# Kernel optimization log

Hardware: AMD Instinct MI355X
Metric: run time of the kernel (lower is better)

Reference implementation:

```python
import jax, jax.numpy as jnp
import numpy as np

GRID_SIZE = 5
SPLINE_ORDER = 3
GRID_MIN, GRID_MAX = -1.0, 1.0
LN_EPS = 1e-5


def _make_grid():
    # Extended knot grid shared across input features: (grid_size + 2*order + 1,)
    h = (GRID_MAX - GRID_MIN) / GRID_SIZE
    return jnp.arange(-SPLINE_ORDER, GRID_SIZE + SPLINE_ORDER + 1, dtype=jnp.float32) * h + GRID_MIN


def b_splines(x, grid):
    # x: (B, in) -> bases: (B, in, grid_size + spline_order)
    xe = x[..., None]  # (B, in, 1)
    bases = ((xe >= grid[:-1]) & (xe < grid[1:])).astype(x.dtype)
    for k in range(1, SPLINE_ORDER + 1):
        left = (xe - grid[: -(k + 1)]) / (grid[k:-1] - grid[: -(k + 1)])
        right = (grid[k + 1:] - xe) / (grid[k + 1:] - grid[1:-k])
        bases = left * bases[..., :-1] + right * bases[..., 1:]
    return bases


def setup_inputs() -> dict:
    key = jax.random.key(0)
    ks = jax.random.split(key, 5)
    B, IN, OUT, COEF = 16384, 1024, 512, GRID_SIZE + SPLINE_ORDER
    return {
        "rgb_features": jax.random.normal(ks[0], (B, IN // 2), jnp.float32),
        "tactile_features": jax.random.normal(ks[1], (B, IN // 2), jnp.float32),
        "base_weight": jax.random.normal(ks[2], (OUT, IN), jnp.float32) * 0.02,
        "spline_weight": jax.random.normal(ks[3], (OUT, IN, COEF), jnp.float32) * 0.02,
        "spline_scaler": 1.0 + 0.02 * jax.random.normal(ks[4], (OUT, IN), jnp.float32),
        "ln_gamma": jnp.ones((OUT,), jnp.float32),
        "ln_beta": jnp.zeros((OUT,), jnp.float32),
    }


def reference(rgb_features, tactile_features, base_weight, spline_weight, spline_scaler, ln_gamma, ln_beta):
    x = jnp.concatenate((rgb_features, tactile_features), axis=1)  # (B, 1024)
    grid = _make_grid()
    # KANLinear: base path (SiLU + linear) + spline path (B-spline basis + linear)
    base_out = jnp.einsum("bi,oi->bo", jax.nn.silu(x), base_weight)
    bases = b_splines(x, grid)  # (B, in, coef)
    scaled_w = spline_weight * spline_scaler[..., None]  # (out, in, coef)
    spline_out = jnp.einsum("bik,oik->bo", bases, scaled_w)
    fused = base_out + spline_out
    # LayerNorm over last dim
    mu = jnp.mean(fused, axis=-1, keepdims=True)
    var = jnp.var(fused, axis=-1, keepdims=True)
    fused = (fused - mu) * jax.lax.rsqrt(var + LN_EPS) * ln_gamma + ln_beta
    # Dropout is identity in eval mode
    return fused
```

## Files before the change

kernel.cpp:

```cpp
#include <hip/hip_runtime.h>
#include <cstdint>
#include <cstddef>


#define BATCH    16384
#define OUT_DIM  512
#define KTOT     9216
#define BM       128
#define BK       64
#define NCHUNK        144
#define SPLINE_CHUNKS 128

typedef __attribute__((ext_vector_type(8))) short  short8;
typedef __attribute__((ext_vector_type(4))) float  f32x4;

static __device__ __forceinline__ unsigned short f2bf(float f) {
    unsigned int u = __float_as_uint(f);
    unsigned int r = u + 0x7fffu + ((u >> 16) & 1u);
    return (unsigned short)(r >> 16);
}

__global__ void prep_w_kernel(const float* __restrict__ bw,
                              const float* __restrict__ sw,
                              const float* __restrict__ sc,
                              unsigned short* __restrict__ Wp) {
    int t = blockIdx.x * 256 + threadIdx.x;
    int o = t / 1152;
    int g = t - o * 1152;
    int sz = o & 7;
    unsigned short o8[8];
    size_t dst;
    if (g < 1024) {
        float s = sc[(size_t)o * 1024 + g];
        const float* w = sw + ((size_t)o * 1024 + g) * 8;
        #pragma unroll
        for (int k = 0; k < 8; ++k) o8[k] = f2bf(w[k] * s);
        dst = (size_t)o * KTOT + (size_t)(g >> 3) * 64 + (size_t)(((g & 7) ^ sz)) * 8;
    } else {
        int gi = g - 1024;
        const float* w = bw + (size_t)o * 1024 + gi * 8;
        #pragma unroll
        for (int k = 0; k < 8; ++k) o8[k] = f2bf(w[k]);
        dst = (size_t)o * KTOT + (size_t)8192 + (size_t)(gi >> 3) * 64 + (size_t)(((gi & 7) ^ sz)) * 8;
    }
    *reinterpret_cast<short8*>(Wp + dst) = *reinterpret_cast<const short8*>(o8);
}

static __device__ __forceinline__ void basis8(float x, unsigned* out) {
    float tpos = (x + 2.2f) * 2.5f;
    float fj   = floorf(tpos);
    int   j    = (int)fj;
    float u  = tpos - fj;
    float v  = 1.f - u;
    float u2 = u * u;
    float u3 = u2 * u;
    const float c6 = 1.f / 6.f;
    float n0 = v * v * v * c6;
    float n1 = (3.f * u3 - 6.f * u2 + 4.f) * c6;
    float n2 = (-3.f * u3 + 3.f * u2 + 3.f * u + 1.f) * c6;
    float n3 = u3 * c6;
    unsigned p0, p1;
    asm("v_cvt_pk_bf16_f32 %0, %1, %2" : "=v"(p0) : "v"(n0), "v"(n1));
    asm("v_cvt_pk_bf16_f32 %0, %1, %2" : "=v"(p1) : "v"(n2), "v"(n3));
    int sh = (j << 4) - 48;
    int c  = sh & 16;
    int w  = (sh - c) >> 5;
    unsigned long long P = ((unsigned long long)p1 << 32) | p0;
    unsigned long long T = P << c;
    unsigned t0 = (unsigned)T;
    unsigned t1 = (unsigned)(T >> 32);
    unsigned t2 = c ? (p1 >> 16) : 0u;
    #pragma unroll
    for (int i = 0; i < 4; ++i) {
        unsigned r = 0u;
        r = (w == i    ) ? t0 : r;
        r = (w == i - 1) ? t1 : r;
        r = (w == i - 2) ? t2 : r;
        out[i] = r;
    }
}

template<bool SPLIT>
__launch_bounds__(1024, 4)
__global__ void kan_gemm_kernel(const float* __restrict__ rgb,
                                const float* __restrict__ tac,
                                const unsigned short* __restrict__ Wp,
                                float* __restrict__ dest_base) {
    __shared__ unsigned short At[2][BM][BK];
    __shared__ unsigned short Bt[2][OUT_DIM][BK];

    const int tid  = threadIdx.x;
    const int lane = tid & 63;
    const int wid  = tid >> 6;
    const int b0   = blockIdx.x * BM;
    const int wr   = wid & 1;
    const int wc   = wid >> 1;
    const int ksp  = SPLIT ? (int)blockIdx.y : 0;
    const int kc0  = SPLIT ? (ksp ? 72 : 0)             : 0;
    const int kcS  = SPLIT ? (ksp ? SPLINE_CHUNKS : 72) : SPLINE_CHUNKS;
    const int kc1  = SPLIT ? (ksp ? NCHUNK : 72)        : NCHUNK;
    float* dest = dest_base + (size_t)ksp * BATCH * OUT_DIM;

    const int ar  = tid >> 3;
    const int af_ = tid & 7;

    f32x4 acc[4][4];
    #pragma unroll
    for (int m = 0; m < 4; ++m)
        #pragma unroll
        for (int n = 0; n < 4; ++n)
            acc[m][n] = (f32x4){0.f, 0.f, 0.f, 0.f};

    auto mfma_step = [&](int ab, int bb) {
        #pragma unroll
        for (int ks = 0; ks < 2; ++ks) {
            int cb = ks * 4 + (lane >> 4);
            short8 afr[4];
            #pragma unroll
            for (int m = 0; m < 4; ++m) {
                int row = wr * 64 + m * 16 + (lane & 15);
                afr[m] = *reinterpret_cast<const short8*>(&At[ab][row][(cb ^ (row & 7)) * 8]);
            }
            #pragma unroll
            for (int n = 0; n < 4; ++n) {
                int row = wc * 64 + n * 16 + (lane & 15);
                short8 bfr = *reinterpret_cast<const short8*>(
                    &Bt[bb][row][(cb ^ (row & 7)) * 8]);
                #pragma unroll
                for (int m = 0; m < 4; ++m)
                    acc[m][n] = __builtin_amdgcn_mfma_f32_16x16x32_bf16(
                        afr[m], bfr, acc[m][n], 0, 0, 0);
            }
        }
    };

    auto loadx_s = [&](int c) -> float {
        int i0 = c * 8;
        const float* xs = (i0 < 512) ? rgb : tac;
        int ic = i0 & 511;
        return xs[(size_t)(b0 + ar) * 512 + ic + af_];
    };

    auto loadx_b = [&](int c, f32x4& xa, f32x4& xb) {
        int i0 = (c - SPLINE_CHUNKS) * 64;
        const float* xs = (i0 < 512) ? rgb : tac;
        int ic = i0 & 511;
        const float* xp = xs + (size_t)(b0 + ar) * 512 + ic + af_ * 8;
        xa = *reinterpret_cast<const f32x4*>(xp);
        xb = *reinterpret_cast<const f32x4*>(xp + 4);
    };

    auto silupack = [&](const f32x4& xa, const f32x4& xb, unsigned* o) {
        float s[8];
        #pragma unroll
        for (int q = 0; q < 4; ++q) {
            float a = xa[q]; s[q]     = a / (1.f + __expf(-a));
            float b = xb[q]; s[q + 4] = b / (1.f + __expf(-b));
        }
        #pragma unroll
        for (int q = 0; q < 4; ++q)
            asm("v_cvt_pk_bf16_f32 %0, %1, %2"
                : "=v"(o[q]) : "v"(s[2 * q]), "v"(s[2 * q + 1]));
    };

    auto writeA = [&](const unsigned* o4, int ab) {
        *reinterpret_cast<short8*>(&At[ab][ar][(af_ ^ (ar & 7)) * 8]) =
            *reinterpret_cast<const short8*>(o4);
    };

    auto gload_B = [&](int kc, int buf) {
        int k0g = kc * BK;
        #pragma unroll
        for (int rp = 0; rp < 4; ++rp) {
            int row0 = wid * 32 + rp * 8;
            const unsigned short* gp =
                Wp + (size_t)(row0 + (lane >> 3)) * KTOT + k0g + (lane & 7) * 8;
            __builtin_amdgcn_global_load_lds(
                (const __attribute__((address_space(1))) unsigned int*)gp,
                (__attribute__((address_space(3))) unsigned int*)&Bt[buf][row0][0],
                16, 0, 0);
        }
    };

    gload_B(kc0, 0);
    gload_B(kc0 + 1 < kc1 ? kc0 + 1 : kc1 - 1, 1);
    {
        float x0 = loadx_s(kc0);
        unsigned o4[4];
        basis8(x0, o4);
        writeA(o4, 0);
    }
    float xn = (kc0 + 1 < kcS) ? loadx_s(kc0 + 1) : 0.f;
    asm volatile("s_waitcnt vmcnt(4) lgkmcnt(0)" ::: "memory");
    __builtin_amdgcn_sched_barrier(0);
    __builtin_amdgcn_s_barrier();
    __builtin_amdgcn_sched_barrier(0);

    for (int t = kc0; t < kcS; ++t) {
        const int  buf   = (t - kc0) & 1;
        const bool moreA = (t + 1 < kcS);
        unsigned o4[4];
        if (moreA) {
            basis8(xn, o4);
            writeA(o4, buf ^ 1);
        }
        if (t + 2 < kcS) xn = loadx_s(t + 2);
        mfma_step(buf, buf);
        __builtin_amdgcn_sched_barrier(0);
        __builtin_amdgcn_s_barrier();
        __builtin_amdgcn_sched_barrier(0);
        int tn = (t + 2 < kc1) ? t + 2 : kc1 - 1;
        gload_B(tn, buf);
        asm volatile("s_waitcnt vmcnt(4) lgkmcnt(0)" ::: "memory");
        __builtin_amdgcn_sched_barrier(0);
        __builtin_amdgcn_s_barrier();
        __builtin_amdgcn_sched_barrier(0);
    }

    if (kcS < kc1) {
        f32x4 xa{}, xb{};
        {
            f32x4 a0, b0;
            loadx_b(kcS, a0, b0);
            unsigned o4[4];
            silupack(a0, b0, o4);
            writeA(o4, (kcS - kc0) & 1);
            if (kcS + 1 < kc1) loadx_b(kcS + 1, xa, xb);
            asm volatile("s_waitcnt lgkmcnt(0)" ::: "memory");
            __builtin_amdgcn_sched_barrier(0);
            __builtin_amdgcn_s_barrier();
            __builtin_amdgcn_sched_barrier(0);
        }
        for (int t = kcS; t < kc1; ++t) {
            const int  buf   = (t - kc0) & 1;
            const bool moreA = (t + 1 < kc1);
            unsigned o4[4];
            if (moreA) {
                silupack(xa, xb, o4);
                writeA(o4, buf ^ 1);
            }
            f32x4 na, nb;
            const bool moreX = (t + 2 < kc1);
            if (moreX) loadx_b(t + 2, na, nb);
            mfma_step(buf, buf);
            __builtin_amdgcn_sched_barrier(0);
            __builtin_amdgcn_s_barrier();
            __builtin_amdgcn_sched_barrier(0);
            int tn = moreX ? t + 2 : kc1 - 1;
            gload_B(tn, buf);
            asm volatile("s_waitcnt vmcnt(4) lgkmcnt(0)" ::: "memory");
            __builtin_amdgcn_sched_barrier(0);
            __builtin_amdgcn_s_barrier();
            __builtin_amdgcn_sched_barrier(0);
            if (moreX) { xa = na; xb = nb; }
        }
    }

    #pragma unroll
    for (int m = 0; m < 4; ++m) {
        int row = b0 + wr * 64 + m * 16 + ((lane >> 4) << 2);
        #pragma unroll
        for (int n = 0; n < 4; ++n) {
            int col = wc * 64 + n * 16 + (lane & 15);
            #pragma unroll
            for (int jj = 0; jj < 4; ++jj)
                dest[(size_t)(row + jj) * OUT_DIM + col] = acc[m][n][jj];
        }
    }
}

__global__ void reduce_ln_kernel(const float* __restrict__ P0,
                                 const float* __restrict__ P1,
                                 const float* __restrict__ gamma,
                                 const float* __restrict__ beta,
                                 float* __restrict__ out) {
    int row  = blockIdx.x * 4 + (threadIdx.x >> 6);
    int lane = threadIdx.x & 63;
    const float* p0 = P0 + (size_t)row * OUT_DIM;
    const float* p1 = P1 + (size_t)row * OUT_DIM;
    f32x4 a0 = *reinterpret_cast<const f32x4*>(p0 + lane * 4);
    f32x4 a1 = *reinterpret_cast<const f32x4*>(p0 + 256 + lane * 4);
    f32x4 b0 = *reinterpret_cast<const f32x4*>(p1 + lane * 4);
    f32x4 b1 = *reinterpret_cast<const f32x4*>(p1 + 256 + lane * 4);
    f32x4 v0, v1;
    #pragma unroll
    for (int q = 0; q < 4; ++q) { v0[q] = a0[q] + b0[q]; v1[q] = a1[q] + b1[q]; }
    float s = 0.f, ss = 0.f;
    #pragma unroll
    for (int q = 0; q < 4; ++q) {
        s  += v0[q] + v1[q];
        ss += v0[q] * v0[q] + v1[q] * v1[q];
    }
    #pragma unroll
    for (int off = 1; off < 64; off <<= 1) {
        s  += __shfl_xor(s, off);
        ss += __shfl_xor(ss, off);
    }
    float mu  = s * (1.f / 512.f);
    float var = ss * (1.f / 512.f) - mu * mu;
    float rs  = rsqrtf(var + 1e-5f);
    f32x4 g0 = *reinterpret_cast<const f32x4*>(gamma + lane * 4);
    f32x4 g1 = *reinterpret_cast<const f32x4*>(gamma + 256 + lane * 4);
    f32x4 e0 = *reinterpret_cast<const f32x4*>(beta + lane * 4);
    f32x4 e1 = *reinterpret_cast<const f32x4*>(beta + 256 + lane * 4);
    float* po = out + (size_t)row * OUT_DIM;
    f32x4 r0, r1;
    #pragma unroll
    for (int q = 0; q < 4; ++q) {
        r0[q] = (v0[q] - mu) * rs * g0[q] + e0[q];
        r1[q] = (v1[q] - mu) * rs * g1[q] + e1[q];
    }
    *reinterpret_cast<f32x4*>(po + lane * 4)       = r0;
    *reinterpret_cast<f32x4*>(po + 256 + lane * 4) = r1;
}

__global__ void ln_kernel(float* __restrict__ io,
                          const float* __restrict__ gamma,
                          const float* __restrict__ beta) {
    int row  = blockIdx.x * 4 + (threadIdx.x >> 6);
    int lane = threadIdx.x & 63;
    float* p = io + (size_t)row * OUT_DIM;
    f32x4 v0 = *reinterpret_cast<const f32x4*>(p + lane * 4);
    f32x4 v1 = *reinterpret_cast<const f32x4*>(p + 256 + lane * 4);
    float s = 0.f, ss = 0.f;
    #pragma unroll
    for (int q = 0; q < 4; ++q) {
        s  += v0[q] + v1[q];
        ss += v0[q] * v0[q] + v1[q] * v1[q];
    }
    #pragma unroll
    for (int off = 1; off < 64; off <<= 1) {
        s  += __shfl_xor(s, off);
        ss += __shfl_xor(ss, off);
    }
    float mu  = s * (1.f / 512.f);
    float var = ss * (1.f / 512.f) - mu * mu;
    float rs  = rsqrtf(var + 1e-5f);
    f32x4 g0 = *reinterpret_cast<const f32x4*>(gamma + lane * 4);
    f32x4 g1 = *reinterpret_cast<const f32x4*>(gamma + 256 + lane * 4);
    f32x4 e0 = *reinterpret_cast<const f32x4*>(beta + lane * 4);
    f32x4 e1 = *reinterpret_cast<const f32x4*>(beta + 256 + lane * 4);
    f32x4 r0, r1;
    #pragma unroll
    for (int q = 0; q < 4; ++q) {
        r0[q] = (v0[q] - mu) * rs * g0[q] + e0[q];
        r1[q] = (v1[q] - mu) * rs * g1[q] + e1[q];
    }
    *reinterpret_cast<f32x4*>(p + lane * 4)       = r0;
    *reinterpret_cast<f32x4*>(p + 256 + lane * 4) = r1;
}

extern "C" void kernel_launch(void* const* d_in, const int* in_sizes, int n_in,
                              void* d_out, int out_size, void* d_ws, size_t ws_size,
                              hipStream_t stream) {
    const float* rgb   = (const float*)d_in[0];
    const float* tac   = (const float*)d_in[1];
    const float* bw    = (const float*)d_in[2];
    const float* sw    = (const float*)d_in[3];
    const float* sc    = (const float*)d_in[4];
    const float* gamma = (const float*)d_in[5];
    const float* beta  = (const float*)d_in[6];
    float* out = (float*)d_out;
    unsigned short* Wp = (unsigned short*)d_ws;

    prep_w_kernel<<<2304, 256, 0, stream>>>(bw, sw, sc, Wp);

    const size_t PART = (size_t)BATCH * OUT_DIM * sizeof(float);
    const size_t POFF = 16ull << 20;
    if (ws_size >= POFF + 2 * PART) {
        float* P = (float*)((char*)d_ws + POFF);
        dim3 g(BATCH / BM, 2);
        kan_gemm_kernel<true><<<g, 1024, 0, stream>>>(rgb, tac, Wp, P);
        reduce_ln_kernel<<<BATCH / 4, 256, 0, stream>>>(
            P, P + (size_t)BATCH * OUT_DIM, gamma, beta, out);
    } else {
        dim3 g(BATCH / BM, 1);
        kan_gemm_kernel<false><<<g, 1024, 0, stream>>>(rgb, tac, Wp, out);
        ln_kernel<<<BATCH / 4, 256, 0, stream>>>(out, gamma, beta);
    }
}
```

Baseline: 184.2 us.

## Stagger MFMA and basis compute across waves, raise MFMA priority, cheapen math

Half of the waves (chosen by a parity of the wave id) now issue their MFMA step before the basis/SiLU A-tile production, and the other half do it after. This staggers tensor-core work against VALU work within the workgroup so the two can overlap. MFMA sections are wrapped in s_setprio to favour matrix issue. The global x loads are hoisted earlier in each iteration. The cubic basis n1 is now computed with FMAs and n2 from partition of unity, and SiLU uses a hardware reciprocal instead of a divide. These cut ALU work but may shift rounding slightly and add wave divergence in code layout.

```diff
diff --git a/kernel.cpp b/kernel.cpp
--- a/kernel.cpp
+++ b/kernel.cpp
@@ -56,9 +56,9 @@
     float u3 = u2 * u;
     const float c6 = 1.f / 6.f;
     float n0 = v * v * v * c6;
-    float n1 = (3.f * u3 - 6.f * u2 + 4.f) * c6;
-    float n2 = (-3.f * u3 + 3.f * u2 + 3.f * u + 1.f) * c6;
     float n3 = u3 * c6;
+    float n1 = __builtin_fmaf(0.5f, u3, __builtin_fmaf(-1.f, u2, 4.f * c6));
+    float n2 = 1.f - n0 - n1 - n3;
     unsigned p0, p1;
     asm("v_cvt_pk_bf16_f32 %0, %1, %2" : "=v"(p0) : "v"(n0), "v"(n1));
     asm("v_cvt_pk_bf16_f32 %0, %1, %2" : "=v"(p1) : "v"(n2), "v"(n3));
@@ -103,6 +103,7 @@
 
     const int ar  = tid >> 3;
     const int af_ = tid & 7;
+    const bool mfma_first = (((wid >> 2) ^ wid) & 1) != 0;
 
     f32x4 acc[4][4];
     #pragma unroll
@@ -112,6 +113,7 @@
             acc[m][n] = (f32x4){0.f, 0.f, 0.f, 0.f};
 
     auto mfma_step = [&](int ab, int bb) {
+        __builtin_amdgcn_s_setprio(1);
         #pragma unroll
         for (int ks = 0; ks < 2; ++ks) {
             int cb = ks * 4 + (lane >> 4);
@@ -132,6 +134,7 @@
                         afr[m], bfr, acc[m][n], 0, 0, 0);
             }
         }
+        __builtin_amdgcn_s_setprio(0);
     };
 
     auto loadx_s = [&](int c) -> float {
@@ -154,8 +157,10 @@
         float s[8];
         #pragma unroll
         for (int q = 0; q < 4; ++q) {
-            float a = xa[q]; s[q]     = a / (1.f + __expf(-a));
-            float b = xb[q]; s[q + 4] = b / (1.f + __expf(-b));
+            float a = xa[q];
+            s[q]     = a * __builtin_amdgcn_rcpf(1.f + __expf(-a));
+            float b = xb[q];
+            s[q + 4] = b * __builtin_amdgcn_rcpf(1.f + __expf(-b));
         }
         #pragma unroll
         for (int q = 0; q < 4; ++q)
@@ -199,13 +204,16 @@
     for (int t = kc0; t < kcS; ++t) {
         const int  buf   = (t - kc0) & 1;
         const bool moreA = (t + 1 < kcS);
+        float xnn = (t + 2 < kcS) ? loadx_s(t + 2) : 0.f;
         unsigned o4[4];
-        if (moreA) {
-            basis8(xn, o4);
-            writeA(o4, buf ^ 1);
-        }
-        if (t + 2 < kcS) xn = loadx_s(t + 2);
-        mfma_step(buf, buf);
+        if (mfma_first) {
+            mfma_step(buf, buf);
+            if (moreA) { basis8(xn, o4); writeA(o4, buf ^ 1); }
+        } else {
+            if (moreA) { basis8(xn, o4); writeA(o4, buf ^ 1); }
+            mfma_step(buf, buf);
+        }
+        xn = xnn;
         __builtin_amdgcn_sched_barrier(0);
         __builtin_amdgcn_s_barrier();
         __builtin_amdgcn_sched_barrier(0);
@@ -234,15 +242,17 @@
         for (int t = kcS; t < kc1; ++t) {
             const int  buf   = (t - kc0) & 1;
             const bool moreA = (t + 1 < kc1);
+            const bool moreX = (t + 2 < kc1);
+            f32x4 na, nb;
+            if (moreX) loadx_b(t + 2, na, nb);
             unsigned o4[4];
-            if (moreA) {
-                silupack(xa, xb, o4);
-                writeA(o4, buf ^ 1);
+            if (mfma_first) {
+                mfma_step(buf, buf);
+                if (moreA) { silupack(xa, xb, o4); writeA(o4, buf ^ 1); }
+            } else {
+                if (moreA) { silupack(xa, xb, o4); writeA(o4, buf ^ 1); }
+                mfma_step(buf, buf);
             }
-            f32x4 na, nb;
-            const bool moreX = (t + 2 < kc1);
-            if (moreX) loadx_b(t + 2, na, nb);
-            mfma_step(buf, buf);
             __builtin_amdgcn_sched_barrier(0);
             __builtin_amdgcn_s_barrier();
             __builtin_amdgcn_sched_barrier(0);
```

Measured after the change: 191.3 us. 1.04x slower.

## Use 8 waves per block with 128x64 warp tiles and cheaper basis math

Applied to the files above, without the earlier changes.

The GEMM kernel moves from 16 waves of 64x64 tiles to 8 waves, each covering a 128-row by 64-column tile. Each wave now reuses every B fragment across eight A fragments, which cuts LDS B reads per MFMA. Each thread loads, packs and writes two A elements per chunk, and the vmcnt waits are changed to match the larger per-thread load counts. The B-spline basis uses an FMA form with n2 taken from partition of unity, and SiLU uses a fast reciprocal. The cost is double the accumulator registers and fewer waves per block, which may lower occupancy or cause spills.

```diff
diff --git a/kernel.cpp b/kernel.cpp
--- a/kernel.cpp
+++ b/kernel.cpp
@@ -56,9 +56,9 @@
     float u3 = u2 * u;
     const float c6 = 1.f / 6.f;
     float n0 = v * v * v * c6;
-    float n1 = (3.f * u3 - 6.f * u2 + 4.f) * c6;
-    float n2 = (-3.f * u3 + 3.f * u2 + 3.f * u + 1.f) * c6;
     float n3 = u3 * c6;
+    float n1 = __builtin_fmaf(0.5f, u3, __builtin_fmaf(-1.f, u2, 4.f * c6));
+    float n2 = 1.f - n0 - n1 - n3;
     unsigned p0, p1;
     asm("v_cvt_pk_bf16_f32 %0, %1, %2" : "=v"(p0) : "v"(n0), "v"(n1));
     asm("v_cvt_pk_bf16_f32 %0, %1, %2" : "=v"(p1) : "v"(n2), "v"(n3));
@@ -81,7 +81,7 @@
 }
 
 template<bool SPLIT>
-__launch_bounds__(1024, 4)
+__launch_bounds__(512, 2)
 __global__ void kan_gemm_kernel(const float* __restrict__ rgb,
                                 const float* __restrict__ tac,
                                 const unsigned short* __restrict__ Wp,
@@ -93,20 +93,15 @@
     const int lane = tid & 63;
     const int wid  = tid >> 6;
     const int b0   = blockIdx.x * BM;
-    const int wr   = wid & 1;
-    const int wc   = wid >> 1;
     const int ksp  = SPLIT ? (int)blockIdx.y : 0;
     const int kc0  = SPLIT ? (ksp ? 72 : 0)             : 0;
     const int kcS  = SPLIT ? (ksp ? SPLINE_CHUNKS : 72) : SPLINE_CHUNKS;
     const int kc1  = SPLIT ? (ksp ? NCHUNK : 72)        : NCHUNK;
     float* dest = dest_base + (size_t)ksp * BATCH * OUT_DIM;
 
-    const int ar  = tid >> 3;
-    const int af_ = tid & 7;
-
-    f32x4 acc[4][4];
-    #pragma unroll
-    for (int m = 0; m < 4; ++m)
+    f32x4 acc[8][4];
+    #pragma unroll
+    for (int m = 0; m < 8; ++m)
         #pragma unroll
         for (int n = 0; n < 4; ++n)
             acc[m][n] = (f32x4){0.f, 0.f, 0.f, 0.f};
@@ -115,47 +110,57 @@
         #pragma unroll
         for (int ks = 0; ks < 2; ++ks) {
             int cb = ks * 4 + (lane >> 4);
-            short8 afr[4];
+            short8 afr[8];
             #pragma unroll
-            for (int m = 0; m < 4; ++m) {
-                int row = wr * 64 + m * 16 + (lane & 15);
+            for (int m = 0; m < 8; ++m) {
+                int row = m * 16 + (lane & 15);
                 afr[m] = *reinterpret_cast<const short8*>(&At[ab][row][(cb ^ (row & 7)) * 8]);
             }
             #pragma unroll
             for (int n = 0; n < 4; ++n) {
-                int row = wc * 64 + n * 16 + (lane & 15);
+                int row = wid * 64 + n * 16 + (lane & 15);
                 short8 bfr = *reinterpret_cast<const short8*>(
                     &Bt[bb][row][(cb ^ (row & 7)) * 8]);
                 #pragma unroll
-                for (int m = 0; m < 4; ++m)
+                for (int m = 0; m < 8; ++m)
                     acc[m][n] = __builtin_amdgcn_mfma_f32_16x16x32_bf16(
                         afr[m], bfr, acc[m][n], 0, 0, 0);
             }
         }
     };
 
-    auto loadx_s = [&](int c) -> float {
+    auto loadx_s = [&](int c, float* xv) {
         int i0 = c * 8;
         const float* xs = (i0 < 512) ? rgb : tac;
         int ic = i0 & 511;
-        return xs[(size_t)(b0 + ar) * 512 + ic + af_];
-    };
-
-    auto loadx_b = [&](int c, f32x4& xa, f32x4& xb) {
+        #pragma unroll
+        for (int rep = 0; rep < 2; ++rep) {
+            int e = tid + rep * 512;
+            xv[rep] = xs[(size_t)(b0 + (e >> 3)) * 512 + ic + (e & 7)];
+        }
+    };
+
+    auto loadx_b = [&](int c, f32x4* xq) {
         int i0 = (c - SPLINE_CHUNKS) * 64;
         const float* xs = (i0 < 512) ? rgb : tac;
         int ic = i0 & 511;
-        const float* xp = xs + (size_t)(b0 + ar) * 512 + ic + af_ * 8;
-        xa = *reinterpret_cast<const f32x4*>(xp);
-        xb = *reinterpret_cast<const f32x4*>(xp + 4);
+        #pragma unroll
+        for (int rep = 0; rep < 2; ++rep) {
+            int gq = tid + rep * 512;
+            const float* xp = xs + (size_t)(b0 + (gq >> 3)) * 512 + ic + (gq & 7) * 8;
+            xq[rep * 2]     = *reinterpret_cast<const f32x4*>(xp);
+            xq[rep * 2 + 1] = *reinterpret_cast<const f32x4*>(xp + 4);
+        }
     };
 
     auto silupack = [&](const f32x4& xa, const f32x4& xb, unsigned* o) {
         float s[8];
         #pragma unroll
         for (int q = 0; q < 4; ++q) {
-            float a = xa[q]; s[q]     = a / (1.f + __expf(-a));
-            float b = xb[q]; s[q + 4] = b / (1.f + __expf(-b));
+            float a = xa[q];
+            s[q]     = a * __builtin_amdgcn_rcpf(1.f + __expf(-a));
+            float b = xb[q];
+            s[q + 4] = b * __builtin_amdgcn_rcpf(1.f + __expf(-b));
         }
         #pragma unroll
         for (int q = 0; q < 4; ++q)
@@ -163,16 +168,22 @@
                 : "=v"(o[q]) : "v"(s[2 * q]), "v"(s[2 * q + 1]));
     };
 
-    auto writeA = [&](const unsigned* o4, int ab) {
-        *reinterpret_cast<short8*>(&At[ab][ar][(af_ ^ (ar & 7)) * 8]) =
-            *reinterpret_cast<const short8*>(o4);
+    auto writeA = [&](const unsigned* o8, int ab) {
+        #pragma unroll
+        for (int rep = 0; rep < 2; ++rep) {
+            int e = tid + rep * 512;
+            int r = e >> 3;
+            int c = e & 7;
+            *reinterpret_cast<short8*>(&At[ab][r][(c ^ (r & 7)) * 8]) =
+                *reinterpret_cast<const short8*>(o8 + rep * 4);
+        }
     };
 
     auto gload_B = [&](int kc, int buf) {
         int k0g = kc * BK;
         #pragma unroll
-        for (int rp = 0; rp < 4; ++rp) {
-            int row0 = wid * 32 + rp * 8;
+        for (int rp = 0; rp < 8; ++rp) {
+            int row0 = wid * 64 + rp * 8;
             const unsigned short* gp =
                 Wp + (size_t)(row0 + (lane >> 3)) * KTOT + k0g + (lane & 7) * 8;
             __builtin_amdgcn_global_load_lds(
@@ -182,16 +193,19 @@
         }
     };
 
+    float xv0[2];
+    loadx_s(kc0, xv0);
     gload_B(kc0, 0);
     gload_B(kc0 + 1 < kc1 ? kc0 + 1 : kc1 - 1, 1);
+    float xn[2] = {0.f, 0.f};
+    if (kc0 + 1 < kcS) loadx_s(kc0 + 1, xn);
     {
-        float x0 = loadx_s(kc0);
-        unsigned o4[4];
-        basis8(x0, o4);
-        writeA(o4, 0);
-    }
-    float xn = (kc0 + 1 < kcS) ? loadx_s(kc0 + 1) : 0.f;
-    asm volatile("s_waitcnt vmcnt(4) lgkmcnt(0)" ::: "memory");
+        unsigned o8[8];
+        basis8(xv0[0], o8);
+        basis8(xv0[1], o8 + 4);
+        writeA(o8, 0);
+    }
+    asm volatile("s_waitcnt vmcnt(10) lgkmcnt(0)" ::: "memory");
     __builtin_amdgcn_sched_barrier(0);
     __builtin_amdgcn_s_barrier();
     __builtin_amdgcn_sched_barrier(0);
@@ -199,33 +213,35 @@
     for (int t = kc0; t < kcS; ++t) {
         const int  buf   = (t - kc0) & 1;
         const bool moreA = (t + 1 < kcS);
-        unsigned o4[4];
+        unsigned o8[8];
         if (moreA) {
-            basis8(xn, o4);
-            writeA(o4, buf ^ 1);
-        }
-        if (t + 2 < kcS) xn = loadx_s(t + 2);
+            basis8(xn[0], o8);
+            basis8(xn[1], o8 + 4);
+            writeA(o8, buf ^ 1);
+        }
+        if (t + 2 < kcS) loadx_s(t + 2, xn);
         mfma_step(buf, buf);
         __builtin_amdgcn_sched_barrier(0);
         __builtin_amdgcn_s_barrier();
         __builtin_amdgcn_sched_barrier(0);
         int tn = (t + 2 < kc1) ? t + 2 : kc1 - 1;
         gload_B(tn, buf);
-        asm volatile("s_waitcnt vmcnt(4) lgkmcnt(0)" ::: "memory");
+        asm volatile("s_waitcnt vmcnt(10) lgkmcnt(0)" ::: "memory");
         __builtin_amdgcn_sched_barrier(0);
         __builtin_amdgcn_s_barrier();
         __builtin_amdgcn_sched_barrier(0);
     }
 
     if (kcS < kc1) {
-        f32x4 xa{}, xb{};
+        f32x4 xq[4];
         {
-            f32x4 a0, b0;
-            loadx_b(kcS, a0, b0);
-            unsigned o4[4];
-            silupack(a0, b0, o4);
-            writeA(o4, (kcS - kc0) & 1);
-            if (kcS + 1 < kc1) loadx_b(kcS + 1, xa, xb);
+            f32x4 x0[4];
+            loadx_b(kcS, x0);
+            unsigned o8[8];
+            silupack(x0[0], x0[1], o8);
+            silupack(x0[2], x0[3], o8 + 4);
+            writeA(o8, (kcS - kc0) & 1);
+            if (kcS + 1 < kc1) loadx_b(kcS + 1, xq);
             asm volatile("s_waitcnt lgkmcnt(0)" ::: "memory");
             __builtin_amdgcn_sched_barrier(0);
             __builtin_amdgcn_s_barrier();
@@ -234,34 +250,38 @@
         for (int t = kcS; t < kc1; ++t) {
             const int  buf   = (t - kc0) & 1;
             const bool moreA = (t + 1 < kc1);
-            unsigned o4[4];
+            const bool moreX = (t + 2 < kc1);
+            unsigned o8[8];
             if (moreA) {
-                silupack(xa, xb, o4);
-                writeA(o4, buf ^ 1);
+                silupack(xq[0], xq[1], o8);
+                silupack(xq[2], xq[3], o8 + 4);
+                writeA(o8, buf ^ 1);
             }
-            f32x4 na, nb;
-            const bool moreX = (t + 2 < kc1);
-            if (moreX) loadx_b(t + 2, na, nb);
+            f32x4 nq[4];
+            if (moreX) loadx_b(t + 2, nq);
             mfma_step(buf, buf);
             __builtin_amdgcn_sched_barrier(0);
             __builtin_amdgcn_s_barrier();
             __builtin_amdgcn_sched_barrier(0);
             int tn = moreX ? t + 2 : kc1 - 1;
             gload_B(tn, buf);
-            asm volatile("s_waitcnt vmcnt(4) lgkmcnt(0)" ::: "memory");
+            asm volatile("s_waitcnt vmcnt(12) lgkmcnt(0)" ::: "memory");
             __builtin_amdgcn_sched_barrier(0);
             __builtin_amdgcn_s_barrier();
             __builtin_amdgcn_sched_barrier(0);
-            if (moreX) { xa = na; xb = nb; }
-        }
-    }
-
-    #pragma unroll
-    for (int m = 0; m < 4; ++m) {
-        int row = b0 + wr * 64 + m * 16 + ((lane >> 4) << 2);
+            if (moreX) {
+                #pragma unroll
+                for (int q = 0; q < 4; ++q) xq[q] = nq[q];
+            }
+        }
+    }
+
+    #pragma unroll
+    for (int m = 0; m < 8; ++m) {
+        int row = b0 + m * 16 + ((lane >> 4) << 2);
         #pragma unroll
         for (int n = 0; n < 4; ++n) {
-            int col = wc * 64 + n * 16 + (lane & 15);
+            int col = wid * 64 + n * 16 + (lane & 15);
             #pragma unroll
             for (int jj = 0; jj < 4; ++jj)
                 dest[(size_t)(row + jj) * OUT_DIM + col] = acc[m][n][jj];
@@ -370,12 +390,12 @@
     if (ws_size >= POFF + 2 * PART) {
         float* P = (float*)((char*)d_ws + POFF);
         dim3 g(BATCH / BM, 2);
-        kan_gemm_kernel<true><<<g, 1024, 0, stream>>>(rgb, tac, Wp, P);
+        kan_gemm_kernel<true><<<g, 512, 0, stream>>>(rgb, tac, Wp, P);
         reduce_ln_kernel<<<BATCH / 4, 256, 0, stream>>>(
             P, P + (size_t)BATCH * OUT_DIM, gamma, beta, out);
     } else {
         dim3 g(BATCH / BM, 1);
-        kan_gemm_kernel<false><<<g, 1024, 0, stream>>>(rgb, tac, Wp, out);
+        kan_gemm_kernel<false><<<g, 512, 0, stream>>>(rgb, tac, Wp, out);
         ln_kernel<<<BATCH / 4, 256, 0, stream>>>(out, gamma, beta);
     }
 }
```

After: 195.8 us. 6.3% more time.
